# Performance work log

Measured on AMD Instinct MI355X. Metric: run time of the kernel, lower is better.

Reference implementation:

```python
import jax, jax.numpy as jnp
import numpy as np

B, C, E = 4, 2048, 1024
H, D = 16, 64

def setup_inputs() -> dict:
    key = jax.random.key(0)
    kx, kq, kk, kv, ko = jax.random.split(key, 5)
    s = 1.0 / np.sqrt(E)
    return {
        "x": jax.random.normal(kx, (B, C, E), dtype=jnp.float32),
        "W_q": jax.random.uniform(kq, (E, H * D), jnp.float32, -s, s),
        "W_k": jax.random.uniform(kk, (E, H * D), jnp.float32, -s, s),
        "W_v": jax.random.uniform(kv, (E, H * D), jnp.float32, -s, s),
        "W_o": jax.random.uniform(ko, (H * D, E), jnp.float32, -s, s),
    }

def reference(x, W_q, W_k, W_v, W_o):
    b, c, e = x.shape
    # project and split heads: [B, H, C, D]
    q = (x @ W_q).reshape(b, c, H, D).transpose(0, 2, 1, 3)
    k = (x @ W_k).reshape(b, c, H, D).transpose(0, 2, 1, 3)
    v = (x @ W_v).reshape(b, c, H, D).transpose(0, 2, 1, 3)
    scores = jnp.einsum('bhqd,bhkd->bhqk', q, k) / jnp.sqrt(jnp.float32(D))
    causal = jnp.tril(jnp.ones((c, c), dtype=bool))
    scores = jnp.where(causal, scores, -jnp.inf)
    weights = jax.nn.softmax(scores, axis=-1)
    hidden = jnp.einsum('bhqk,bhkd->bhqd', weights, v)
    hidden = hidden.transpose(0, 2, 1, 3).reshape(b, c, H * D)
    return hidden @ W_o
```

## Files before the change

### kernel.cpp

```cpp
#include <hip/hip_runtime.h>
#include <hip/hip_bf16.h>


typedef __attribute__((ext_vector_type(8))) short short8;
typedef __attribute__((ext_vector_type(4))) float floatx4;
typedef __attribute__((ext_vector_type(4))) unsigned short ushort4v;

extern "C" __device__ float __ocml_exp2_f32(float);

__device__ __forceinline__ unsigned short f2bf(float f) {
    __hip_bfloat16 h = __float2bfloat16(f);
    return __builtin_bit_cast(unsigned short, h);
}

__device__ __forceinline__ void gl2lds16(const unsigned short* g, unsigned short* l) {
    __builtin_amdgcn_global_load_lds(
        (const __attribute__((address_space(1))) unsigned int*)g,
        (__attribute__((address_space(3))) unsigned int*)l, 16, 0, 0);
}

__global__ __launch_bounds__(256) void f2bf_kernel(const float* __restrict__ src,
                                                   unsigned short* __restrict__ dst,
                                                   int n4) {
    int i = blockIdx.x * blockDim.x + threadIdx.x;
    if (i < n4) {
        const float4 v = ((const float4*)src)[i];
        ushort4v o;
        o[0] = f2bf(v.x); o[1] = f2bf(v.y); o[2] = f2bf(v.z); o[3] = f2bf(v.w);
        ((ushort4v*)dst)[i] = o;
    }
}

__global__ __launch_bounds__(256) void transcvt4_kernel(const float* __restrict__ W0,
                                                        const float* __restrict__ W1,
                                                        const float* __restrict__ W2,
                                                        const float* __restrict__ W3,
                                                        unsigned short* __restrict__ dst) {
    const int z = blockIdx.z;
    const float* src = (z == 0) ? W0 : (z == 1) ? W1 : (z == 2) ? W2 : W3;
    const float scale = (z == 0) ? 0.18033688011112042f : 1.0f;
    dst += (size_t)z * 1048576;
    __shared__ float tile[64][65];
    const int t = threadIdx.x;
    const int k0 = blockIdx.y * 64, n0 = blockIdx.x * 64;
    const int r = t >> 4, c4 = (t & 15) * 4;
    #pragma unroll
    for (int p = 0; p < 4; ++p) {
        const int kk = p * 16 + r;
        const float4 v = *(const float4*)&src[(size_t)(k0 + kk) * 1024 + n0 + c4];
        tile[kk][c4 + 0] = v.x; tile[kk][c4 + 1] = v.y;
        tile[kk][c4 + 2] = v.z; tile[kk][c4 + 3] = v.w;
    }
    __syncthreads();
    #pragma unroll
    for (int p = 0; p < 4; ++p) {
        const int nn = p * 16 + r;
        ushort4v o;
        #pragma unroll
        for (int j = 0; j < 4; ++j) o[j] = f2bf(tile[c4 + j][nn] * scale);
        *(ushort4v*)&dst[(size_t)(n0 + nn) * 1024 + k0 + c4] = o;
    }
}

template<int MODE, int NBLK>
__global__ __launch_bounds__(256) void gemm128(const unsigned short* __restrict__ A,
                                               const unsigned short* __restrict__ Bt,
                                               unsigned short* __restrict__ obf,
                                               float* __restrict__ ofp) {
    constexpr int Kd = 1024;
    __shared__ __align__(16) unsigned short Al[128 * 64];
    __shared__ __align__(16) unsigned short Bl[128 * 64];
    const int id = blockIdx.x;
    const int xcd = id & 7;
    const int q = id >> 3;
    const int m_blk = xcd * 8 + (q & 7);
    const int n_blk = q >> 3;
    const int m0 = m_blk * 128, n0 = n_blk * 128;

    const int tid = threadIdx.x;
    const int lane = tid & 63, w = tid >> 6;
    const int quad = lane >> 4, l15 = lane & 15;
    const int wm = (w & 1) * 64, wn = (w >> 1) * 64;
    const int srow = lane >> 3, sc = lane & 7;
    const int gc = (sc ^ srow) * 8;

    floatx4 acc[4][4];
    #pragma unroll
    for (int i = 0; i < 4; ++i)
        #pragma unroll
        for (int j = 0; j < 4; ++j) acc[i][j] = (floatx4){0.f, 0.f, 0.f, 0.f};

    for (int kt = 0; kt < Kd / 64; ++kt) {
        const int k0 = kt * 64;
        #pragma unroll
        for (int p = 0; p < 4; ++p) {
            const int row0 = w * 32 + p * 8;
            gl2lds16(&A[(size_t)(m0 + row0 + srow) * Kd + k0 + gc], &Al[row0 * 64]);
            gl2lds16(&Bt[(size_t)(n0 + row0 + srow) * Kd + k0 + gc], &Bl[row0 * 64]);
        }
        __syncthreads();
        #pragma unroll
        for (int kk = 0; kk < 2; ++kk) {
            short8 af[4], bfv[4];
            #pragma unroll
            for (int i = 0; i < 4; ++i) {
                const int row = wm + i * 16 + l15;
                af[i] = *(const short8*)&Al[row * 64 + ((kk * 4 + quad) ^ (row & 7)) * 8];
            }
            #pragma unroll
            for (int i = 0; i < 4; ++i) {
                const int row = wn + i * 16 + l15;
                bfv[i] = *(const short8*)&Bl[row * 64 + ((kk * 4 + quad) ^ (row & 7)) * 8];
            }
            #pragma unroll
            for (int i = 0; i < 4; ++i)
                #pragma unroll
                for (int j = 0; j < 4; ++j)
                    acc[i][j] = __builtin_amdgcn_mfma_f32_16x16x32_bf16(
                        af[i], bfv[j], acc[i][j], 0, 0, 0);
        }
        __syncthreads();
    }

    #pragma unroll
    for (int i = 0; i < 4; ++i) {
        if (MODE == 0 && n0 >= 2048) {
            #pragma unroll
            for (int j = 0; j < 4; ++j) {
                const int mb = m0 + wm + i * 16 + quad * 4;
                const int n = n0 + wn + j * 16 + l15;
                const int b = mb >> 11, c0 = mb & 2047;
                const int nl = n & 1023, hh = nl >> 6, d = nl & 63;
                ushort4v pv;
                #pragma unroll
                for (int r = 0; r < 4; ++r) pv[r] = f2bf(acc[i][j][r]);
                *(ushort4v*)&obf[16777216 + ((size_t)(b * 16 + hh) * 64 + d) * 2048 + c0] = pv;
            }
        } else {
            #pragma unroll
            for (int r = 0; r < 4; ++r) {
                const int m = m0 + wm + i * 16 + quad * 4 + r;
                #pragma unroll
                for (int j = 0; j < 4; ++j) {
                    const int n = n0 + wn + j * 16 + l15;
                    const float v = acc[i][j][r];
                    if (MODE == 0) {
                        const int b = m >> 11, c = m & 2047;
                        const int z = n >> 10, nl = n & 1023, hh = nl >> 6, d = nl & 63;
                        obf[(size_t)z * 8388608 +
                            ((size_t)(b * 16 + hh) * 2048 + c) * 64 + d] = f2bf(v);
                    } else {
                        ofp[(size_t)m * 1024 + n] = v;
                    }
                }
            }
        }
    }
}

__global__ __launch_bounds__(512) void attn_kernel(const unsigned short* __restrict__ Q,
                                                   const unsigned short* __restrict__ K,
                                                   const unsigned short* __restrict__ Vt,
                                                   unsigned short* __restrict__ Hid) {
    __shared__ __align__(16) unsigned short Kl[64 * 64];
    __shared__ __align__(16) unsigned short Vl[64 * 64];
    __shared__ __align__(16) unsigned short Pl[8][16 * 72];
    const int id = blockIdx.x;
    const int bh = (id >> 6) * 8 + (id & 7);
    const int xq = (id >> 3) & 7;
    const int b = bh >> 4, h = bh & 15;
    const int tid = threadIdx.x, w = tid >> 6, lane = tid & 63;
    const int quad = lane >> 4, l15 = lane & 15;
    const int sw = quad ^ (l15 & 7);
    const int srow = lane >> 3, sc = lane & 7;
    const size_t bhs = (size_t)(b * 16 + h) * 2048 * 64;
    const unsigned short* Qb = Q + bhs;
    const unsigned short* Kb = K + bhs;
    const unsigned short* Vb = Vt + bhs;

    #pragma unroll
    for (int pass = 0; pass < 2; ++pass) {
        const int qt = pass ? (15 - xq) : xq;
        const int q0 = qt * 128;
        const int qw = q0 + w * 16;
        const int myq = qw + l15;
        const short8 bq0 = *(const short8*)&Qb[(size_t)myq * 64 + quad * 8];
        const short8 bq1 = *(const short8*)&Qb[(size_t)myq * 64 + 32 + quad * 8];

        floatx4 o[4];
        #pragma unroll
        for (int i = 0; i < 4; ++i) o[i] = (floatx4){0.f, 0.f, 0.f, 0.f};
        float li = 0.f;

        const int nT = (q0 + 128) >> 6;
        for (int t = 0; t < nT; ++t) {
            const int k0 = t * 64;
            {
                const int krow = w * 8 + srow;
                const int g8 = (sc ^ srow) * 8;
                gl2lds16(&Kb[(size_t)(k0 + krow) * 64 + g8], &Kl[w * 512]);
                gl2lds16(&Vb[(size_t)krow * 2048 + k0 + g8], &Vl[w * 512]);
            }
            __syncthreads();
            if (k0 <= qw + 15) {
                floatx4 s[4];
                #pragma unroll
                for (int kf = 0; kf < 4; ++kf) {
                    const int row = kf * 16 + l15;
                    const short8 ka0 = *(const short8*)&Kl[row * 64 + sw * 8];
                    const short8 ka1 = *(const short8*)&Kl[row * 64 + (sw ^ 4) * 8];
                    floatx4 ss = (floatx4){0.f, 0.f, 0.f, 0.f};
                    ss = __builtin_amdgcn_mfma_f32_16x16x32_bf16(ka0, bq0, ss, 0, 0, 0);
                    ss = __builtin_amdgcn_mfma_f32_16x16x32_bf16(ka1, bq1, ss, 0, 0, 0);
                    s[kf] = ss;
                }
                if (k0 + 63 > qw) {
                    #pragma unroll
                    for (int kf = 0; kf < 4; ++kf) {
                        ushort4v pw;
                        #pragma unroll
                        for (int r = 0; r < 4; ++r) {
                            const int key = k0 + kf * 16 + quad * 4 + r;
                            const float p = (key > myq) ? 0.f : __ocml_exp2_f32(s[kf][r]);
                            li += p;
                            pw[r] = f2bf(p);
                        }
                        *(ushort4v*)&Pl[w][l15 * 72 + kf * 16 + quad * 4] = pw;
                    }
                } else {
                    #pragma unroll
                    for (int kf = 0; kf < 4; ++kf) {
                        ushort4v pw;
                        #pragma unroll
                        for (int r = 0; r < 4; ++r) {
                            const float p = __ocml_exp2_f32(s[kf][r]);
                            li += p;
                            pw[r] = f2bf(p);
                        }
                        *(ushort4v*)&Pl[w][l15 * 72 + kf * 16 + quad * 4] = pw;
                    }
                }
                __threadfence_block();
                const short8 pb0 = *(const short8*)&Pl[w][l15 * 72 + quad * 8];
                const short8 pb1 = *(const short8*)&Pl[w][l15 * 72 + 32 + quad * 8];
                #pragma unroll
                for (int nt = 0; nt < 4; ++nt) {
                    const int row = nt * 16 + l15;
                    const short8 va0 = *(const short8*)&Vl[row * 64 + sw * 8];
                    const short8 va1 = *(const short8*)&Vl[row * 64 + (sw ^ 4) * 8];
                    floatx4 oo = o[nt];
                    oo = __builtin_amdgcn_mfma_f32_16x16x32_bf16(va0, pb0, oo, 0, 0, 0);
                    oo = __builtin_amdgcn_mfma_f32_16x16x32_bf16(va1, pb1, oo, 0, 0, 0);
                    o[nt] = oo;
                }
            }
            __syncthreads();
        }

        li += __shfl_xor(li, 16, 64);
        li += __shfl_xor(li, 32, 64);
        const float inv = 1.f / li;
        #pragma unroll
        for (int nt = 0; nt < 4; ++nt) {
            ushort4v ov;
            #pragma unroll
            for (int r = 0; r < 4; ++r) ov[r] = f2bf(o[nt][r] * inv);
            *(ushort4v*)&Hid[((size_t)b * 2048 + myq) * 1024 + h * 64 + nt * 16 + quad * 4] = ov;
        }
    }
}

extern "C" void kernel_launch(void* const* d_in, const int* in_sizes, int n_in,
                              void* d_out, int out_size, void* d_ws, size_t ws_size,
                              hipStream_t stream) {
    const float* x  = (const float*)d_in[0];
    const float* Wq = (const float*)d_in[1];
    const float* Wk = (const float*)d_in[2];
    const float* Wv = (const float*)d_in[3];
    const float* Wo = (const float*)d_in[4];
    float* out = (float*)d_out;
    unsigned short* ws = (unsigned short*)d_ws;

    const size_t XB  = 0;
    const size_t WQT = 8388608;
    const size_t QO  = 12582912;
    const size_t HO  = 37748736;

    f2bf_kernel<<<8192, 256, 0, stream>>>(x, ws + XB, 2097152);
    transcvt4_kernel<<<dim3(16, 16, 4), 256, 0, stream>>>(Wq, Wk, Wv, Wo, ws + WQT);

    gemm128<0, 24><<<1536, 256, 0, stream>>>(ws + XB, ws + WQT, ws + QO, nullptr);
    attn_kernel<<<512, 512, 0, stream>>>(ws + QO, ws + QO + 8388608,
                                         ws + QO + 16777216, ws + HO);
    gemm128<1, 8><<<512, 256, 0, stream>>>(ws + HO, ws + WQT + 3145728, nullptr, out);
}
```

Measured before the change: 247.6 us.

## Merge prep kernels and shrink attention q-tile to 64 rows with 4 waves

```diff
diff --git a/kernel.cpp b/kernel.cpp
--- a/kernel.cpp
+++ b/kernel.cpp
@@ -19,30 +19,30 @@
         (__attribute__((address_space(3))) unsigned int*)l, 16, 0, 0);
 }
 
-__global__ __launch_bounds__(256) void f2bf_kernel(const float* __restrict__ src,
-                                                   unsigned short* __restrict__ dst,
-                                                   int n4) {
-    int i = blockIdx.x * blockDim.x + threadIdx.x;
-    if (i < n4) {
-        const float4 v = ((const float4*)src)[i];
+__global__ __launch_bounds__(256) void prep_kernel(const float* __restrict__ x,
+                                                   const float* __restrict__ W0,
+                                                   const float* __restrict__ W1,
+                                                   const float* __restrict__ W2,
+                                                   const float* __restrict__ W3,
+                                                   unsigned short* __restrict__ xb,
+                                                   unsigned short* __restrict__ wt) {
+    __shared__ float tile[64][65];
+    const int id = blockIdx.x;
+    if (id < 8192) {
+        const int i = id * 256 + threadIdx.x;
+        const float4 v = ((const float4*)x)[i];
         ushort4v o;
         o[0] = f2bf(v.x); o[1] = f2bf(v.y); o[2] = f2bf(v.z); o[3] = f2bf(v.w);
-        ((ushort4v*)dst)[i] = o;
-    }
-}
-
-__global__ __launch_bounds__(256) void transcvt4_kernel(const float* __restrict__ W0,
-                                                        const float* __restrict__ W1,
-                                                        const float* __restrict__ W2,
-                                                        const float* __restrict__ W3,
-                                                        unsigned short* __restrict__ dst) {
-    const int z = blockIdx.z;
+        ((ushort4v*)xb)[i] = o;
+        return;
+    }
+    const int t2 = id - 8192;
+    const int z = t2 >> 8;
     const float* src = (z == 0) ? W0 : (z == 1) ? W1 : (z == 2) ? W2 : W3;
     const float scale = (z == 0) ? 0.18033688011112042f : 1.0f;
-    dst += (size_t)z * 1048576;
-    __shared__ float tile[64][65];
+    unsigned short* dst = wt + (size_t)z * 1048576;
+    const int k0 = ((t2 >> 4) & 15) * 64, n0 = (t2 & 15) * 64;
     const int t = threadIdx.x;
-    const int k0 = blockIdx.y * 64, n0 = blockIdx.x * 64;
     const int r = t >> 4, c4 = (t & 15) * 4;
     #pragma unroll
     for (int p = 0; p < 4; ++p) {
@@ -158,21 +158,22 @@
     }
 }
 
-__global__ __launch_bounds__(512) void attn_kernel(const unsigned short* __restrict__ Q,
+__global__ __launch_bounds__(256) void attn_kernel(const unsigned short* __restrict__ Q,
                                                    const unsigned short* __restrict__ K,
                                                    const unsigned short* __restrict__ Vt,
                                                    unsigned short* __restrict__ Hid) {
     __shared__ __align__(16) unsigned short Kl[64 * 64];
     __shared__ __align__(16) unsigned short Vl[64 * 64];
-    __shared__ __align__(16) unsigned short Pl[8][16 * 72];
+    __shared__ __align__(16) unsigned short Pl[4][16 * 72];
     const int id = blockIdx.x;
-    const int bh = (id >> 6) * 8 + (id & 7);
-    const int xq = (id >> 3) & 7;
+    const int bh = (id >> 7) * 8 + (id & 7);
+    const int xq = (id >> 3) & 15;
     const int b = bh >> 4, h = bh & 15;
     const int tid = threadIdx.x, w = tid >> 6, lane = tid & 63;
     const int quad = lane >> 4, l15 = lane & 15;
     const int sw = quad ^ (l15 & 7);
     const int srow = lane >> 3, sc = lane & 7;
+    const int g8 = (sc ^ srow) * 8;
     const size_t bhs = (size_t)(b * 16 + h) * 2048 * 64;
     const unsigned short* Qb = Q + bhs;
     const unsigned short* Kb = K + bhs;
@@ -180,8 +181,8 @@
 
     #pragma unroll
     for (int pass = 0; pass < 2; ++pass) {
-        const int qt = pass ? (15 - xq) : xq;
-        const int q0 = qt * 128;
+        const int qt = pass ? (31 - xq) : xq;
+        const int q0 = qt * 64;
         const int qw = q0 + w * 16;
         const int myq = qw + l15;
         const short8 bq0 = *(const short8*)&Qb[(size_t)myq * 64 + quad * 8];
@@ -192,14 +193,16 @@
         for (int i = 0; i < 4; ++i) o[i] = (floatx4){0.f, 0.f, 0.f, 0.f};
         float li = 0.f;
 
-        const int nT = (q0 + 128) >> 6;
+        const int nT = (q0 + 64) >> 6;
         for (int t = 0; t < nT; ++t) {
             const int k0 = t * 64;
             {
-                const int krow = w * 8 + srow;
-                const int g8 = (sc ^ srow) * 8;
-                gl2lds16(&Kb[(size_t)(k0 + krow) * 64 + g8], &Kl[w * 512]);
-                gl2lds16(&Vb[(size_t)krow * 2048 + k0 + g8], &Vl[w * 512]);
+                #pragma unroll
+                for (int p = 0; p < 2; ++p) {
+                    const int row0 = p * 32 + w * 8;
+                    gl2lds16(&Kb[(size_t)(k0 + row0 + srow) * 64 + g8], &Kl[row0 * 64]);
+                    gl2lds16(&Vb[(size_t)(row0 + srow) * 2048 + k0 + g8], &Vl[row0 * 64]);
+                }
             }
             __syncthreads();
             if (k0 <= qw + 15) {
@@ -286,11 +289,10 @@
     const size_t QO  = 12582912;
     const size_t HO  = 37748736;
 
-    f2bf_kernel<<<8192, 256, 0, stream>>>(x, ws + XB, 2097152);
-    transcvt4_kernel<<<dim3(16, 16, 4), 256, 0, stream>>>(Wq, Wk, Wv, Wo, ws + WQT);
+    prep_kernel<<<9216, 256, 0, stream>>>(x, Wq, Wk, Wv, Wo, ws + XB, ws + WQT);
 
     gemm128<0, 24><<<1536, 256, 0, stream>>>(ws + XB, ws + WQT, ws + QO, nullptr);
-    attn_kernel<<<512, 512, 0, stream>>>(ws + QO, ws + QO + 8388608,
-                                         ws + QO + 16777216, ws + HO);
+    attn_kernel<<<1024, 256, 0, stream>>>(ws + QO, ws + QO + 8388608,
+                                          ws + QO + 16777216, ws + HO);
     gemm128<1, 8><<<512, 256, 0, stream>>>(ws + HO, ws + WQT + 3145728, nullptr, out);
 }
```

Measured after the change: 253.1 us. 2.2% more time.
